# Kernel optimization log

Hardware: AMD Instinct MI355X
Metric: run time of the kernel (lower is better)

## Reference

```python
import jax, jax.numpy as jnp
import numpy as np

B, T, L = 512, 512, 64

def setup_inputs() -> dict:
    key = jax.random.key(0)
    k1, k2, k3, k4, k5 = jax.random.split(key, 5)
    emission = jax.random.normal(k1, (B, T, L), dtype=jnp.float32)
    target = jax.random.randint(k2, (B, T), 0, L, dtype=jnp.int32)
    mask = jnp.ones((B, T), dtype=jnp.float32)
    start_trans = jax.random.uniform(k3, (L,), minval=-0.1, maxval=0.1, dtype=jnp.float32)
    trans = jax.random.uniform(k4, (L, L), minval=-0.1, maxval=0.1, dtype=jnp.float32)
    end_trans = jax.random.uniform(k5, (L,), minval=-0.1, maxval=0.1, dtype=jnp.float32)
    return {"emission": emission, "target": target, "mask": mask,
            "start_trans": start_trans, "trans": trans, "end_trans": end_trans}


def _crf_nll(emission, target, mask, start_trans, trans, end_trans):
    # end_mask: 1 at the last valid position of each sequence
    left_shift = jnp.concatenate([mask[:, 1:], jnp.zeros_like(mask[:, :1])], axis=1)
    end_mask = (mask > left_shift).astype(emission.dtype)  # [B,T]

    em_t = jnp.swapaxes(emission, 0, 1)   # [T,B,L]
    mask_t = mask.T                       # [T,B]
    endm_t = end_mask.T                   # [T,B]
    tgt_t = target.T                      # [T,B]
    brange = jnp.arange(emission.shape[0])

    # ---- normalizer: log-space forward algorithm over time ----
    init_scores = start_trans + em_t[0]   # [B,L]

    def norm_step(scores, xs):
        em_i, m_i, e_i = xs
        nxt = jax.scipy.special.logsumexp(scores[:, :, None] + trans, axis=1) + em_i
        m = m_i[:, None]
        nxt = m * nxt + (1.0 - m) * scores
        nxt = nxt + e_i[:, None] * end_trans
        return nxt, None

    scores, _ = jax.lax.scan(norm_step, init_scores, (em_t[1:], mask_t[1:], endm_t[1:]))
    normalizer = jax.scipy.special.logsumexp(scores, axis=1)  # [B]

    # ---- gold path score ----
    ps0 = start_trans[tgt_t[0]] + em_t[0][brange, tgt_t[0]]   # [B]

    def path_step(carry, xs):
        ps, prev = carry
        em_i, m_i, e_i, t_i = xs
        nxt = ps + trans[prev, t_i] + em_i[brange, t_i]
        nxt = m_i * nxt + (1.0 - m_i) * ps
        nxt = nxt + e_i * end_trans[t_i]
        return (nxt, t_i), None

    (path_scores, _), _ = jax.lax.scan(
        path_step, (ps0, tgt_t[0]), (em_t[1:], mask_t[1:], endm_t[1:], tgt_t[1:]))

    return jnp.mean(normalizer - path_scores)


def reference(emission, target, mask, start_trans, trans, end_trans):
    return _crf_nll(emission, target, mask, start_trans, trans, end_trans)
```

## Files before the change

### kernel.cpp

```cpp
#include <hip/hip_runtime.h>

#define NB 512
#define NT 512
#define NL 64
#define L2E 1.4426950408889634f
#define LN2 0.6931471805599453f

typedef _Float16 h2 __attribute__((ext_vector_type(2)));
typedef _Float16 h8 __attribute__((ext_vector_type(8)));

__global__ void zero_out_kernel(float* out) { *out = 0.0f; }

__device__ __forceinline__ float dot2f(h2 a, h2 b, float c) {
#if __has_builtin(__builtin_amdgcn_fdot2)
  return __builtin_amdgcn_fdot2(a, b, c, false);
#else
  return fmaf((float)a[0], (float)b[0], fmaf((float)a[1], (float)b[1], c));
#endif
}

__global__
__attribute__((amdgpu_flat_work_group_size(128, 128), amdgpu_waves_per_eu(1, 1)))
void crf_nll_kernel(
    const float* __restrict__ emission,
    const int*   __restrict__ target,
    const float* __restrict__ mask,
    const float* __restrict__ start_trans,
    const float* __restrict__ trans,
    const float* __restrict__ end_trans,
    float* __restrict__ out)
{
  const int b = blockIdx.x;
  const int tid = threadIdx.x;
  const int wv = tid >> 6;
  const int j = tid & 63;

  const float* em_b = emission + (size_t)b * NT * NL;
  const float* mk_b = mask + (size_t)b * NT;
  const int*   tg_b = target + (size_t)b * NT;

  __shared__ __align__(16) _Float16 qF[NL];
  __shared__ __align__(16) _Float16 qB[NL];
  __shared__ float fF[NL], fB[NL];
  __shared__ float psS[2];
  __shared__ int   GS[2];

  float ps = 0.0f;
  #pragma unroll
  for (int c = 4 * wv; c < 4 * wv + 4; ++c) {
    int t = c * 64 + j;
    int cur = tg_b[t];
    float m  = mk_b[t];
    float mn = (t + 1 < NT) ? mk_b[t + 1] : 0.0f;
    if (t == 0) {
      ps += start_trans[cur] + em_b[cur];
    } else {
      int prev = tg_b[t - 1];
      if (m > 0.5f)
        ps += trans[prev * NL + cur] + em_b[(size_t)t * NL + cur];
      if (m - mn > 0.5f)
        ps += end_trans[cur];
    }
  }
  #pragma unroll
  for (int off = 32; off; off >>= 1) ps += __shfl_down(ps, off, 64);

  const float endt = __builtin_amdgcn_exp2f(L2E * end_trans[j]);

  int G = 0;
  float s;

  if (wv == 0) {
    h2 ep[NL / 2];
    #pragma unroll
    for (int k = 0; k < NL / 2; ++k) {
      float e0 = __builtin_amdgcn_exp2f(L2E * trans[(2 * k + 0) * NL + j]);
      float e1 = __builtin_amdgcn_exp2f(L2E * trans[(2 * k + 1) * NL + j]);
      h2 v; v[0] = (_Float16)e0; v[1] = (_Float16)e1;
      ep[k] = v;
    }
    s = __builtin_amdgcn_exp2f(L2E * (start_trans[j] + em_b[j]));
    qF[j] = (_Float16)s;
    const h8* qv = (const h8*)qF;

    float pf[8];
    #pragma unroll
    for (int u = 0; u < 8; ++u) pf[u] = L2E * em_b[(size_t)u * NL + j];

    #pragma unroll 1
    for (int c = 0; c < 4; ++c) {
      const int tb = c * 64;
      float ml = mk_b[tb + j];
      int nidx = tb + j + 1;
      float mnext = (nidx < NT) ? mk_b[nidx] : 0.0f;
      unsigned long long cm = __ballot(ml > 0.5f);
      unsigned long long ce = __ballot(ml - mnext > 0.5f);
      if (c == 0) { cm &= ~1ull; ce &= ~1ull; }

      #pragma unroll 1
      for (int i8 = 0; i8 < 64; i8 += 8) {
        #pragma unroll
        for (int u = 0; u < 8; ++u) {
          const int i = i8 + u;
          float eemu = __builtin_amdgcn_exp2f(pf[u]);
          eemu = ((ce >> i) & 1) ? eemu * endt : eemu;
          int tp = tb + i + 8; if (tp > NT - 1) tp = NT - 1;
          pf[u] = L2E * em_b[(size_t)tp * NL + j];
          float a0 = 0.f, a1 = 0.f, a2 = 0.f, a3 = 0.f;
          float a4 = 0.f, a5 = 0.f, a6 = 0.f, a7 = 0.f;
          #pragma unroll
          for (int k = 0; k < 8; ++k) {
            h8 x = qv[k];
            h2 x0 = __builtin_shufflevector(x, x, 0, 1);
            h2 x1 = __builtin_shufflevector(x, x, 2, 3);
            h2 x2 = __builtin_shufflevector(x, x, 4, 5);
            h2 x3 = __builtin_shufflevector(x, x, 6, 7);
            if (k & 1) {
              a4 = dot2f(x0, ep[4 * k + 0], a4);
              a5 = dot2f(x1, ep[4 * k + 1], a5);
              a6 = dot2f(x2, ep[4 * k + 2], a6);
              a7 = dot2f(x3, ep[4 * k + 3], a7);
            } else {
              a0 = dot2f(x0, ep[4 * k + 0], a0);
              a1 = dot2f(x1, ep[4 * k + 1], a1);
              a2 = dot2f(x2, ep[4 * k + 2], a2);
              a3 = dot2f(x3, ep[4 * k + 3], a3);
            }
          }
          float sm = (((a0 + a4) + (a1 + a5)) + ((a2 + a6) + (a3 + a7)));
          unsigned e0 =
            (__builtin_amdgcn_readfirstlane(__float_as_uint(sm)) >> 23) & 0xffu;
          float scale = __uint_as_float((254u - e0) << 23);
          float snew = (sm * scale) * eemu;
          float sold = s * scale;
          s = ((cm >> i) & 1) ? snew : sold;
          qF[j] = (_Float16)s;
          G += (int)e0 - 127;
        }
      }
    }
  } else {
    h2 epb[NL / 2];
    const float4* trow = (const float4*)(trans + (size_t)j * NL);
    #pragma unroll
    for (int k4 = 0; k4 < 16; ++k4) {
      float4 v4 = trow[k4];
      h2 p0; p0[0] = (_Float16)__builtin_amdgcn_exp2f(L2E * v4.x);
             p0[1] = (_Float16)__builtin_amdgcn_exp2f(L2E * v4.y);
      h2 p1; p1[0] = (_Float16)__builtin_amdgcn_exp2f(L2E * v4.z);
             p1[1] = (_Float16)__builtin_amdgcn_exp2f(L2E * v4.w);
      epb[2 * k4 + 0] = p0;
      epb[2 * k4 + 1] = p1;
    }
    s = 1.0f;
    const h8* qv = (const h8*)qB;

    float pf[8];
    #pragma unroll
    for (int u = 0; u < 8; ++u) pf[u] = L2E * em_b[(size_t)(504 + u) * NL + j];

    #pragma unroll 1
    for (int c = 7; c >= 4; --c) {
      const int tb = c * 64;
      float ml = mk_b[tb + j];
      int nidx = tb + j + 1;
      float mnext = (nidx < NT) ? mk_b[nidx] : 0.0f;
      unsigned long long cm = __ballot(ml > 0.5f);
      unsigned long long ce = __ballot(ml - mnext > 0.5f);

      #pragma unroll 1
      for (int i8 = 56; i8 >= 0; i8 -= 8) {
        #pragma unroll
        for (int u = 7; u >= 0; --u) {
          const int i = i8 + u;
          const int t = tb + i;
          float eemu = __builtin_amdgcn_exp2f(pf[u]);
          float wmul = ((cm >> i) & 1) ? eemu : 1.0f;
          wmul = ((ce >> i) & 1) ? wmul * endt : wmul;
          int tp = t - 8; if (tp < 0) tp = 0;
          pf[u] = L2E * em_b[(size_t)tp * NL + j];
          float w = s * wmul;
          if ((cm >> i) & 1) {
            qB[j] = (_Float16)w;
            float a0 = 0.f, a1 = 0.f, a2 = 0.f, a3 = 0.f;
            float a4 = 0.f, a5 = 0.f, a6 = 0.f, a7 = 0.f;
            #pragma unroll
            for (int k = 0; k < 8; ++k) {
              h8 x = qv[k];
              h2 x0 = __builtin_shufflevector(x, x, 0, 1);
              h2 x1 = __builtin_shufflevector(x, x, 2, 3);
              h2 x2 = __builtin_shufflevector(x, x, 4, 5);
              h2 x3 = __builtin_shufflevector(x, x, 6, 7);
              if (k & 1) {
                a4 = dot2f(x0, epb[4 * k + 0], a4);
                a5 = dot2f(x1, epb[4 * k + 1], a5);
                a6 = dot2f(x2, epb[4 * k + 2], a6);
                a7 = dot2f(x3, epb[4 * k + 3], a7);
              } else {
                a0 = dot2f(x0, epb[4 * k + 0], a0);
                a1 = dot2f(x1, epb[4 * k + 1], a1);
                a2 = dot2f(x2, epb[4 * k + 2], a2);
                a3 = dot2f(x3, epb[4 * k + 3], a3);
              }
            }
            float sm = (((a0 + a4) + (a1 + a5)) + ((a2 + a6) + (a3 + a7)));
            unsigned e0 =
              (__builtin_amdgcn_readfirstlane(__float_as_uint(sm)) >> 23) & 0xffu;
            float scale = __uint_as_float((254u - e0) << 23);
            s = sm * scale;
            G += (int)e0 - 127;
          } else {
            s = w;
          }
        }
      }
    }
  }

  if (wv == 0) { fF[j] = s; if (j == 0) { psS[0] = ps; GS[0] = G; } }
  else         { fB[j] = s; if (j == 0) { psS[1] = ps; GS[1] = G; } }
  __syncthreads();
  if (wv == 0) {
    float prod = s * fB[j];
    #pragma unroll
    for (int off = 32; off; off >>= 1) prod += __shfl_xor(prod, off, 64);
    if (j == 0) {
      float norm = (__builtin_amdgcn_logf(prod) + (float)(GS[0] + GS[1])) * LN2;
      atomicAdd(out, (norm - psS[0] - psS[1]) * (1.0f / (float)NB));
    }
  }
}

extern "C" void kernel_launch(void* const* d_in, const int* in_sizes, int n_in,
                              void* d_out, int out_size, void* d_ws, size_t ws_size,
                              hipStream_t stream) {
  const float* emission    = (const float*)d_in[0];
  const int*   target      = (const int*)  d_in[1];
  const float* mask        = (const float*)d_in[2];
  const float* start_trans = (const float*)d_in[3];
  const float* trans       = (const float*)d_in[4];
  const float* end_trans   = (const float*)d_in[5];
  float* out = (float*)d_out;

  zero_out_kernel<<<1, 1, 0, stream>>>(out);
  crf_nll_kernel<<<NB, 128, 0, stream>>>(emission, target, mask, start_trans,
                                         trans, end_trans, out);
}
```

Before: 159.3 us.

## Replace LDS-based state broadcast with DPP/swizzle cross-lane matvec

The per-step 64x64 matrix-vector product no longer writes the state vector to shared memory and reads it back as h8 vectors. Each lane now packs fp16 state pairs and exchanges them through DPP moves and ds_swizzle. It computes partial dot products over a 16x16 tile, and reduces across the four row groups with xor shuffles. The exp(trans) register layout is re-arranged to match. The aim is to cut LDS store/load latency and the implicit sync on the serial recurrence's critical path, at the cost of more cross-lane ops and extra shuffle latency per step.

After: 173.6 us. 1.09x slower.

```diff
diff --git a/kernel.cpp b/kernel.cpp
--- a/kernel.cpp
+++ b/kernel.cpp
@@ -7,7 +7,6 @@
 #define LN2 0.6931471805599453f
 
 typedef _Float16 h2 __attribute__((ext_vector_type(2)));
-typedef _Float16 h8 __attribute__((ext_vector_type(8)));
 
 __global__ void zero_out_kernel(float* out) { *out = 0.0f; }
 
@@ -17,6 +16,44 @@
 #else
   return fmaf((float)a[0], (float)b[0], fmaf((float)a[1], (float)b[1], c));
 #endif
+}
+
+__device__ __forceinline__ h2 bch2(unsigned u) { return __builtin_bit_cast(h2, u); }
+
+__device__ __forceinline__ float matvec64(float hval, const h2 (&ep)[4][8],
+                                          bool rb0, bool rb1) {
+  unsigned hu = (unsigned)__builtin_bit_cast(unsigned short, (_Float16)hval);
+  unsigned n1 = (unsigned)__builtin_amdgcn_mov_dpp((int)hu, 0xB1, 0xF, 0xF, true);
+  unsigned p0 = hu | (n1 << 16);
+  unsigned p1 = (unsigned)__builtin_amdgcn_mov_dpp((int)p0, 0x4E, 0xF, 0xF, true);
+  unsigned p2 = (unsigned)__builtin_amdgcn_ds_swizzle((int)p0, 0x101F);
+  unsigned p3 = (unsigned)__builtin_amdgcn_ds_swizzle((int)p1, 0x101F);
+  unsigned p4 = (unsigned)__builtin_amdgcn_ds_swizzle((int)p0, 0x201F);
+  unsigned p5 = (unsigned)__builtin_amdgcn_ds_swizzle((int)p1, 0x201F);
+  unsigned p6 = (unsigned)__builtin_amdgcn_ds_swizzle((int)p2, 0x201F);
+  unsigned p7 = (unsigned)__builtin_amdgcn_ds_swizzle((int)p3, 0x201F);
+  float P[4];
+#pragma unroll
+  for (int q = 0; q < 4; ++q) {
+    float a = dot2f(bch2(p0), ep[q][0], 0.0f);
+    a = dot2f(bch2(p1), ep[q][1], a);
+    a = dot2f(bch2(p2), ep[q][2], a);
+    a = dot2f(bch2(p3), ep[q][3], a);
+    float bq = dot2f(bch2(p4), ep[q][4], 0.0f);
+    bq = dot2f(bch2(p5), ep[q][5], bq);
+    bq = dot2f(bch2(p6), ep[q][6], bq);
+    bq = dot2f(bch2(p7), ep[q][7], bq);
+    P[q] = a + bq;
+  }
+  float qa = rb0 ? P[1] : P[0];
+  float sa = rb0 ? P[0] : P[1];
+  float qb = rb0 ? P[3] : P[2];
+  float sb = rb0 ? P[2] : P[3];
+  qa += __shfl_xor(sa, 16, 64);
+  qb += __shfl_xor(sb, 16, 64);
+  float qq = rb1 ? qb : qa;
+  float ss = rb1 ? qa : qb;
+  return qq + __shfl_xor(ss, 32, 64);
 }
 
 __global__
@@ -34,21 +71,23 @@
   const int tid = threadIdx.x;
   const int wv = tid >> 6;
   const int j = tid & 63;
+  const int r = j >> 4;
+  const int c = j & 15;
+  const bool rb0 = (r & 1) != 0;
+  const bool rb1 = (r & 2) != 0;
 
   const float* em_b = emission + (size_t)b * NT * NL;
   const float* mk_b = mask + (size_t)b * NT;
   const int*   tg_b = target + (size_t)b * NT;
 
-  __shared__ __align__(16) _Float16 qF[NL];
-  __shared__ __align__(16) _Float16 qB[NL];
   __shared__ float fF[NL], fB[NL];
   __shared__ float psS[2];
   __shared__ int   GS[2];
 
   float ps = 0.0f;
   #pragma unroll
-  for (int c = 4 * wv; c < 4 * wv + 4; ++c) {
-    int t = c * 64 + j;
+  for (int cc = 4 * wv; cc < 4 * wv + 4; ++cc) {
+    int t = cc * 64 + j;
     int cur = tg_b[t];
     float m  = mk_b[t];
     float mn = (t + 1 < NT) ? mk_b[t + 1] : 0.0f;
@@ -71,31 +110,35 @@
   float s;
 
   if (wv == 0) {
-    h2 ep[NL / 2];
-    #pragma unroll
-    for (int k = 0; k < NL / 2; ++k) {
-      float e0 = __builtin_amdgcn_exp2f(L2E * trans[(2 * k + 0) * NL + j]);
-      float e1 = __builtin_amdgcn_exp2f(L2E * trans[(2 * k + 1) * NL + j]);
-      h2 v; v[0] = (_Float16)e0; v[1] = (_Float16)e1;
-      ep[k] = v;
+    h2 ep[4][8];
+    #pragma unroll
+    for (int q = 0; q < 4; ++q) {
+      const int col = 16 * q + c;
+      #pragma unroll
+      for (int m = 0; m < 8; ++m) {
+        const int i0 = 16 * r + (c ^ (2 * m));
+        const int i1 = i0 ^ 1;
+        float e0 = __builtin_amdgcn_exp2f(L2E * trans[i0 * NL + col]);
+        float e1 = __builtin_amdgcn_exp2f(L2E * trans[i1 * NL + col]);
+        h2 v; v[0] = (_Float16)e0; v[1] = (_Float16)e1;
+        ep[q][m] = v;
+      }
     }
     s = __builtin_amdgcn_exp2f(L2E * (start_trans[j] + em_b[j]));
-    qF[j] = (_Float16)s;
-    const h8* qv = (const h8*)qF;
 
     float pf[8];
     #pragma unroll
     for (int u = 0; u < 8; ++u) pf[u] = L2E * em_b[(size_t)u * NL + j];
 
     #pragma unroll 1
-    for (int c = 0; c < 4; ++c) {
-      const int tb = c * 64;
+    for (int cc = 0; cc < 4; ++cc) {
+      const int tb = cc * 64;
       float ml = mk_b[tb + j];
       int nidx = tb + j + 1;
       float mnext = (nidx < NT) ? mk_b[nidx] : 0.0f;
       unsigned long long cm = __ballot(ml > 0.5f);
       unsigned long long ce = __ballot(ml - mnext > 0.5f);
-      if (c == 0) { cm &= ~1ull; ce &= ~1ull; }
+      if (cc == 0) { cm &= ~1ull; ce &= ~1ull; }
 
       #pragma unroll 1
       for (int i8 = 0; i8 < 64; i8 += 8) {
@@ -106,62 +149,41 @@
           eemu = ((ce >> i) & 1) ? eemu * endt : eemu;
           int tp = tb + i + 8; if (tp > NT - 1) tp = NT - 1;
           pf[u] = L2E * em_b[(size_t)tp * NL + j];
-          float a0 = 0.f, a1 = 0.f, a2 = 0.f, a3 = 0.f;
-          float a4 = 0.f, a5 = 0.f, a6 = 0.f, a7 = 0.f;
-          #pragma unroll
-          for (int k = 0; k < 8; ++k) {
-            h8 x = qv[k];
-            h2 x0 = __builtin_shufflevector(x, x, 0, 1);
-            h2 x1 = __builtin_shufflevector(x, x, 2, 3);
-            h2 x2 = __builtin_shufflevector(x, x, 4, 5);
-            h2 x3 = __builtin_shufflevector(x, x, 6, 7);
-            if (k & 1) {
-              a4 = dot2f(x0, ep[4 * k + 0], a4);
-              a5 = dot2f(x1, ep[4 * k + 1], a5);
-              a6 = dot2f(x2, ep[4 * k + 2], a6);
-              a7 = dot2f(x3, ep[4 * k + 3], a7);
-            } else {
-              a0 = dot2f(x0, ep[4 * k + 0], a0);
-              a1 = dot2f(x1, ep[4 * k + 1], a1);
-              a2 = dot2f(x2, ep[4 * k + 2], a2);
-              a3 = dot2f(x3, ep[4 * k + 3], a3);
-            }
-          }
-          float sm = (((a0 + a4) + (a1 + a5)) + ((a2 + a6) + (a3 + a7)));
+          float sm = matvec64(s, ep, rb0, rb1);
           unsigned e0 =
             (__builtin_amdgcn_readfirstlane(__float_as_uint(sm)) >> 23) & 0xffu;
           float scale = __uint_as_float((254u - e0) << 23);
           float snew = (sm * scale) * eemu;
           float sold = s * scale;
           s = ((cm >> i) & 1) ? snew : sold;
-          qF[j] = (_Float16)s;
           G += (int)e0 - 127;
         }
       }
     }
   } else {
-    h2 epb[NL / 2];
-    const float4* trow = (const float4*)(trans + (size_t)j * NL);
-    #pragma unroll
-    for (int k4 = 0; k4 < 16; ++k4) {
-      float4 v4 = trow[k4];
-      h2 p0; p0[0] = (_Float16)__builtin_amdgcn_exp2f(L2E * v4.x);
-             p0[1] = (_Float16)__builtin_amdgcn_exp2f(L2E * v4.y);
-      h2 p1; p1[0] = (_Float16)__builtin_amdgcn_exp2f(L2E * v4.z);
-             p1[1] = (_Float16)__builtin_amdgcn_exp2f(L2E * v4.w);
-      epb[2 * k4 + 0] = p0;
-      epb[2 * k4 + 1] = p1;
+    h2 ep[4][8];
+    #pragma unroll
+    for (int q = 0; q < 4; ++q) {
+      const int rowi = 16 * q + c;
+      #pragma unroll
+      for (int m = 0; m < 8; ++m) {
+        const int j0 = 16 * r + (c ^ (2 * m));
+        const int j1 = j0 ^ 1;
+        float e0 = __builtin_amdgcn_exp2f(L2E * trans[rowi * NL + j0]);
+        float e1 = __builtin_amdgcn_exp2f(L2E * trans[rowi * NL + j1]);
+        h2 v; v[0] = (_Float16)e0; v[1] = (_Float16)e1;
+        ep[q][m] = v;
+      }
     }
     s = 1.0f;
-    const h8* qv = (const h8*)qB;
 
     float pf[8];
     #pragma unroll
     for (int u = 0; u < 8; ++u) pf[u] = L2E * em_b[(size_t)(504 + u) * NL + j];
 
     #pragma unroll 1
-    for (int c = 7; c >= 4; --c) {
-      const int tb = c * 64;
+    for (int cc = 7; cc >= 4; --cc) {
+      const int tb = cc * 64;
       float ml = mk_b[tb + j];
       int nidx = tb + j + 1;
       float mnext = (nidx < NT) ? mk_b[nidx] : 0.0f;
@@ -181,29 +203,7 @@
           pf[u] = L2E * em_b[(size_t)tp * NL + j];
           float w = s * wmul;
           if ((cm >> i) & 1) {
-            qB[j] = (_Float16)w;
-            float a0 = 0.f, a1 = 0.f, a2 = 0.f, a3 = 0.f;
-            float a4 = 0.f, a5 = 0.f, a6 = 0.f, a7 = 0.f;
-            #pragma unroll
-            for (int k = 0; k < 8; ++k) {
-              h8 x = qv[k];
-              h2 x0 = __builtin_shufflevector(x, x, 0, 1);
-              h2 x1 = __builtin_shufflevector(x, x, 2, 3);
-              h2 x2 = __builtin_shufflevector(x, x, 4, 5);
-              h2 x3 = __builtin_shufflevector(x, x, 6, 7);
-              if (k & 1) {
-                a4 = dot2f(x0, epb[4 * k + 0], a4);
-                a5 = dot2f(x1, epb[4 * k + 1], a5);
-                a6 = dot2f(x2, epb[4 * k + 2], a6);
-                a7 = dot2f(x3, epb[4 * k + 3], a7);
-              } else {
-                a0 = dot2f(x0, epb[4 * k + 0], a0);
-                a1 = dot2f(x1, epb[4 * k + 1], a1);
-                a2 = dot2f(x2, epb[4 * k + 2], a2);
-                a3 = dot2f(x3, epb[4 * k + 3], a3);
-              }
-            }
-            float sm = (((a0 + a4) + (a1 + a5)) + ((a2 + a6) + (a3 + a7)));
+            float sm = matvec64(w, ep, rb0, rb1);
             unsigned e0 =
               (__builtin_amdgcn_readfirstlane(__float_as_uint(sm)) >> 23) & 0xffu;
             float scale = __uint_as_float((254u - e0) << 23);
```
